# Kernel optimization log

Measured on AMD Instinct MI355X. Metric: run time of the kernel, lower is better.

Reference implementation:

```python
import jax, jax.numpy as jnp
import numpy as np

N = 50000
E = 800000
D_IN = 256
D_OUT = 512
GIN_EPS = 0.0      # eps param, train_eps=False -> constant
BN_EPS = 1e-5      # BatchNorm1d default eps


def setup_inputs() -> dict:
    key = jax.random.key(0)
    ks = jax.random.split(key, 9)
    x = jax.random.normal(ks[0], (N, D_IN), dtype=jnp.float32)
    edge_index = jax.random.randint(ks[1], (2, E), 0, N, dtype=jnp.int32)
    edge_weight = jax.random.uniform(ks[2], (E,), dtype=jnp.float32)
    # MLP params: Linear(D_IN,D_OUT) -> BatchNorm1d(D_OUT) -> ReLU -> Linear(D_OUT,D_OUT)
    s1 = 1.0 / np.sqrt(D_IN)
    s2 = 1.0 / np.sqrt(D_OUT)
    W1 = jax.random.uniform(ks[3], (D_IN, D_OUT), jnp.float32, -s1, s1)
    b1 = jax.random.uniform(ks[4], (D_OUT,), jnp.float32, -s1, s1)
    gamma = jnp.ones((D_OUT,), jnp.float32)
    beta = jnp.zeros((D_OUT,), jnp.float32)
    W2 = jax.random.uniform(ks[5], (D_OUT, D_OUT), jnp.float32, -s2, s2)
    b2 = jax.random.uniform(ks[6], (D_OUT,), jnp.float32, -s2, s2)
    return {"x": x, "edge_index": edge_index, "edge_weight": edge_weight,
            "W1": W1, "b1": b1, "gamma": gamma, "beta": beta, "W2": W2, "b2": b2}


def reference(x, edge_index, edge_weight, W1, b1, gamma, beta, W2, b2):
    row, col = edge_index[0], edge_index[1]
    # gather neighbor features, scale by edge weight, scatter-add into destination rows
    msg = edge_weight[:, None] * x[col]                      # (E, D_IN)
    agg = jax.ops.segment_sum(msg, row, num_segments=x.shape[0])  # (N, D_IN)
    h = (1.0 + GIN_EPS) * x + agg                            # GIN combine
    # MLP: Linear -> BatchNorm1d (training-mode batch stats) -> ReLU -> Linear
    h = h @ W1 + b1                                          # (N, D_OUT)
    mean = jnp.mean(h, axis=0)
    var = jnp.var(h, axis=0)                                 # biased, as torch BN uses
    h = (h - mean) * jax.lax.rsqrt(var + BN_EPS) * gamma + beta
    h = jax.nn.relu(h)
    return h @ W2 + b2
```

## Files before the change

### kernel.cpp

```cpp
#include <hip/hip_runtime.h>

#define NNODES 50000
#define NEDGES 800000
#define DIN    256
#define DOUT   512
#define MP     50048
#define BN_EPS 1e-5f
#define NBLK   196

#define CVT_B  6250
#define ZERO_B 391
#define T1_B   128
#define T2_B   256
#define PREP_B (CVT_B + ZERO_B + T1_B + T2_B)

typedef __attribute__((ext_vector_type(8))) __bf16 bf16x8;
typedef __attribute__((ext_vector_type(4))) float  floatx4;

__device__ __forceinline__ uint pkbf(float a, float b) {
    union { __bf16 h[2]; uint u; } cv;
    cv.h[0] = (__bf16)a; cv.h[1] = (__bf16)b;
    return cv.u;
}
__device__ __forceinline__ ushort f2bf(float f) {
    union { __bf16 h; ushort u; } cv;
    cv.h = (__bf16)f;
    return cv.u;
}
__device__ __forceinline__ float bf2f(ushort b) {
    union { uint u; float f; } v; v.u = ((uint)b) << 16;
    return v.f;
}
__device__ __forceinline__ uint bnpack(uint u, float s0, float s1, float h0, float h1) {
    float a = fmaxf(bf2f((ushort)(u & 0xffff)) * s0 + h0, 0.f);
    float b = fmaxf(bf2f((ushort)(u >> 16))    * s1 + h1, 0.f);
    return pkbf(a, b);
}

__global__ __launch_bounds__(256) void k_prep(const float* __restrict__ x, ushort* __restrict__ xb,
                                              const float* __restrict__ W1, ushort* __restrict__ W1T,
                                              const float* __restrict__ W2, ushort* __restrict__ W2T,
                                              int* __restrict__ zi, float* __restrict__ zf) {
    __shared__ float tile[32][33];
    int b = blockIdx.x;
    int t = threadIdx.x;
    if (b < CVT_B) {
        size_t base = ((size_t)b * 256 + t) * 8;
        float4 v0 = *(const float4*)(x + base);
        float4 v1 = *(const float4*)(x + base + 4);
        uint4 o;
        o.x = pkbf(v0.x, v0.y);
        o.y = pkbf(v0.z, v0.w);
        o.z = pkbf(v1.x, v1.y);
        o.w = pkbf(v1.z, v1.w);
        *(uint4*)(xb + base) = o;
        return;
    }
    b -= CVT_B;
    if (b < ZERO_B) {
        int i = b * 256 + t;
        if (i < 2 * MP) zi[i] = 0;
        if (i < 1024)   zf[i] = 0.f;
        return;
    }
    b -= ZERO_B;
    const float* W; ushort* WT; int K, Nc, bx, by;
    if (b < T1_B) { W = W1; WT = W1T; K = DIN;  Nc = DOUT; bx = b & 15; by = b >> 4; }
    else { b -= T1_B; W = W2; WT = W2T; K = DOUT; Nc = DOUT; bx = b & 15; by = b >> 4; }
    int lx = t & 31, ly = t >> 5;
    #pragma unroll
    for (int p = 0; p < 4; ++p)
        tile[ly + p * 8][lx] = W[(size_t)(by * 32 + ly + p * 8) * Nc + bx * 32 + lx];
    __syncthreads();
    #pragma unroll
    for (int p = 0; p < 4; ++p)
        WT[(size_t)(bx * 32 + ly + p * 8) * K + by * 32 + lx] = f2bf(tile[lx][ly + p * 8]);
}

__global__ void k_count(const int* __restrict__ ei, int* __restrict__ deg) {
    int e = blockIdx.x * 256 + threadIdx.x;
    atomicAdd(&deg[ei[e]], 1);
}

__global__ void k_scan_block(const int* __restrict__ deg, int* __restrict__ rowstart,
                             int* __restrict__ bsum) {
    __shared__ int s[256];
    int t = threadIdx.x;
    int i = blockIdx.x * 256 + t;
    int v = (i < NNODES) ? deg[i] : 0;
    s[t] = v; __syncthreads();
    #pragma unroll
    for (int d = 1; d < 256; d <<= 1) {
        int add = (t >= d) ? s[t - d] : 0;
        __syncthreads();
        s[t] += add;
        __syncthreads();
    }
    if (i < MP) rowstart[i] = s[t] - v;
    if (t == 255) bsum[blockIdx.x] = s[255];
}

__global__ void k_scan_bsum(const int* __restrict__ bsum, int* __restrict__ bofs) {
    __shared__ int s[256];
    int t = threadIdx.x;
    int v = (t < NBLK) ? bsum[t] : 0;
    s[t] = v; __syncthreads();
    #pragma unroll
    for (int d = 1; d < 256; d <<= 1) {
        int add = (t >= d) ? s[t - d] : 0;
        __syncthreads();
        s[t] += add;
        __syncthreads();
    }
    bofs[t] = s[t] - v;
}

__global__ void k_bucket(const int* __restrict__ ei, const float* __restrict__ ew,
                         const int* __restrict__ rowstart, const int* __restrict__ bofs,
                         int* __restrict__ cursor, int2* __restrict__ cw) {
    int e = blockIdx.x * 256 + threadIdx.x;
    int r = ei[e];
    int c = ei[NEDGES + e];
    float w = ew[e];
    int pos = rowstart[r] + bofs[r >> 8] + atomicAdd(&cursor[r], 1);
    cw[pos] = make_int2(c, __float_as_int(w));
}

__global__ __launch_bounds__(256) void k_aggregate(const ushort* __restrict__ xb,
                                                   const int2* __restrict__ cw,
                                                   const int* __restrict__ rowstart,
                                                   const int* __restrict__ bofs,
                                                   const int* __restrict__ deg,
                                                   ushort* __restrict__ h0b) {
    int t = threadIdx.x;
    int wv = t >> 6, lane = t & 63;
    int n = blockIdx.x * 4 + wv;
    if (n >= MP) return;
    ushort* dst = h0b + (size_t)n * DIN + lane * 4;
    if (n >= NNODES) {
        *(ushort4*)dst = make_ushort4(0, 0, 0, 0);
        return;
    }
    const ushort* xl = xb + lane * 4;
    ushort4 sd = *(const ushort4*)(xl + (size_t)n * DIN);
    float4 acc = make_float4(bf2f(sd.x), bf2f(sd.y), bf2f(sd.z), bf2f(sd.w));
    int start = rowstart[n] + bofs[n >> 8];
    int end   = start + deg[n];
    int j = start;
    for (; j + 3 < end; j += 4) {
        int2 e0 = cw[j], e1 = cw[j + 1], e2 = cw[j + 2], e3 = cw[j + 3];
        ushort4 v0 = *(const ushort4*)(xl + (size_t)e0.x * DIN);
        ushort4 v1 = *(const ushort4*)(xl + (size_t)e1.x * DIN);
        ushort4 v2 = *(const ushort4*)(xl + (size_t)e2.x * DIN);
        ushort4 v3 = *(const ushort4*)(xl + (size_t)e3.x * DIN);
        float w0 = __int_as_float(e0.y), w1 = __int_as_float(e1.y);
        float w2 = __int_as_float(e2.y), w3 = __int_as_float(e3.y);
        acc.x += w0 * bf2f(v0.x); acc.y += w0 * bf2f(v0.y); acc.z += w0 * bf2f(v0.z); acc.w += w0 * bf2f(v0.w);
        acc.x += w1 * bf2f(v1.x); acc.y += w1 * bf2f(v1.y); acc.z += w1 * bf2f(v1.z); acc.w += w1 * bf2f(v1.w);
        acc.x += w2 * bf2f(v2.x); acc.y += w2 * bf2f(v2.y); acc.z += w2 * bf2f(v2.z); acc.w += w2 * bf2f(v2.w);
        acc.x += w3 * bf2f(v3.x); acc.y += w3 * bf2f(v3.y); acc.z += w3 * bf2f(v3.z); acc.w += w3 * bf2f(v3.w);
    }
    for (; j < end; ++j) {
        int2 cv = cw[j];
        float w = __int_as_float(cv.y);
        ushort4 v = *(const ushort4*)(xl + (size_t)cv.x * DIN);
        acc.x += w * bf2f(v.x); acc.y += w * bf2f(v.y); acc.z += w * bf2f(v.z); acc.w += w * bf2f(v.w);
    }
    uint2 o;
    o.x = pkbf(acc.x, acc.y);
    o.y = pkbf(acc.z, acc.w);
    *(uint2*)dst = o;
}

template<int KDIM, int MODE>
__global__ __launch_bounds__(256) void k_gemm(const ushort* __restrict__ A,
                                              const ushort* __restrict__ BT,
                                              const float* __restrict__ bias,
                                              const float* __restrict__ scale,
                                              const float* __restrict__ shift,
                                              float* __restrict__ gsum,
                                              float* __restrict__ gsq,
                                              void* __restrict__ out) {
    constexpr int LDSK = 64 + 8;
    __shared__ ushort As[128][LDSK];
    __shared__ ushort Bs[128][LDSK];

    int t    = threadIdx.x;
    int bm   = blockIdx.x >> 2;
    int bn   = blockIdx.x & 3;
    int lane = t & 63;
    int w    = t >> 6;
    int wr   = w >> 1, wc = w & 1;
    int l15  = lane & 15, l4 = lane >> 4;

    floatx4 acc[4][4] = {};

    int arow = t >> 3;
    int acol = (t & 7) * 8;
    const size_t abase = (size_t)(bm * 128) * KDIM;
    const size_t bbase = (size_t)(bn * 128) * KDIM;

    for (int k0 = 0; k0 < KDIM; k0 += 64) {
        float4 sc0, sc1, sh0, sh1;
        if (MODE == 2) {
            sc0 = *(const float4*)(scale + k0 + acol);
            sc1 = *(const float4*)(scale + k0 + acol + 4);
            sh0 = *(const float4*)(shift + k0 + acol);
            sh1 = *(const float4*)(shift + k0 + acol + 4);
        }
        #pragma unroll
        for (int p = 0; p < 4; ++p) {
            int row = p * 32 + arow;
            uint4 va = *(const uint4*)(A  + abase + (size_t)row * KDIM + k0 + acol);
            if (MODE == 2) {
                va.x = bnpack(va.x, sc0.x, sc0.y, sh0.x, sh0.y);
                va.y = bnpack(va.y, sc0.z, sc0.w, sh0.z, sh0.w);
                va.z = bnpack(va.z, sc1.x, sc1.y, sh1.x, sh1.y);
                va.w = bnpack(va.w, sc1.z, sc1.w, sh1.z, sh1.w);
            }
            *(uint4*)&As[row][acol] = va;
            uint4 vb = *(const uint4*)(BT + bbase + (size_t)row * KDIM + k0 + acol);
            *(uint4*)&Bs[row][acol] = vb;
        }
        __syncthreads();
        #pragma unroll
        for (int ks = 0; ks < 2; ++ks) {
            bf16x8 af[4], bfr[4];
            #pragma unroll
            for (int m = 0; m < 4; ++m)
                af[m] = *(const bf16x8*)&As[wr * 64 + m * 16 + l15][ks * 32 + l4 * 8];
            #pragma unroll
            for (int n = 0; n < 4; ++n)
                bfr[n] = *(const bf16x8*)&Bs[wc * 64 + n * 16 + l15][ks * 32 + l4 * 8];
            #pragma unroll
            for (int m = 0; m < 4; ++m)
                #pragma unroll
                for (int n = 0; n < 4; ++n)
                    acc[m][n] = __builtin_amdgcn_mfma_f32_16x16x32_bf16(af[m], bfr[n], acc[m][n], 0, 0, 0);
        }
        __syncthreads();
    }

    float csum[4], csq[4];
    #pragma unroll
    for (int n = 0; n < 4; ++n) { csum[n] = 0.f; csq[n] = 0.f; }

    #pragma unroll
    for (int n = 0; n < 4; ++n) {
        int col = bn * 128 + wc * 64 + n * 16 + l15;
        float bv = bias[col];
        #pragma unroll
        for (int m = 0; m < 4; ++m) {
            int rbase = bm * 128 + wr * 64 + m * 16 + l4 * 4;
            #pragma unroll
            for (int i = 0; i < 4; ++i) {
                int grow = rbase + i;
                float vv = acc[m][n][i] + bv;
                if (MODE == 1) {
                    ((ushort*)out)[(size_t)grow * DOUT + col] = f2bf(vv);
                    if (grow < NNODES) { csum[n] += vv; csq[n] += vv * vv; }
                } else {
                    if (grow < NNODES)
                        ((float*)out)[(size_t)grow * DOUT + col] = vv;
                }
            }
        }
    }

    if (MODE == 1) {
        float* sumarr = (float*)&As[0][0];
        float* sqarr  = sumarr + 1024;
        int cid = wr * 4 + l4;
        #pragma unroll
        for (int n = 0; n < 4; ++n) {
            int colL = wc * 64 + n * 16 + l15;
            sumarr[cid * 128 + colL] = csum[n];
            sqarr [cid * 128 + colL] = csq[n];
        }
        __syncthreads();
        if (t < 128) {
            float s = 0.f, q = 0.f;
            #pragma unroll
            for (int k = 0; k < 8; ++k) { s += sumarr[k * 128 + t]; q += sqarr[k * 128 + t]; }
            atomicAdd(&gsum[bn * 128 + t], s);
            atomicAdd(&gsq [bn * 128 + t], q);
        }
    }
}

__global__ void k_bn_finalize(const float* __restrict__ sum, const float* __restrict__ sumsq,
                              const float* __restrict__ gamma, const float* __restrict__ beta,
                              float* __restrict__ scale, float* __restrict__ shift) {
    int c = threadIdx.x;
    float mean = sum[c] * (1.0f / NNODES);
    float var  = sumsq[c] * (1.0f / NNODES) - mean * mean;
    float sc   = gamma[c] * rsqrtf(var + BN_EPS);
    scale[c] = sc;
    shift[c] = beta[c] - mean * sc;
}

extern "C" void kernel_launch(void* const* d_in, const int* in_sizes, int n_in,
                              void* d_out, int out_size, void* d_ws, size_t ws_size,
                              hipStream_t stream) {
    const float* x     = (const float*)d_in[0];
    const int*   ei    = (const int*)  d_in[1];
    const float* ew    = (const float*)d_in[2];
    const float* W1    = (const float*)d_in[3];
    const float* b1    = (const float*)d_in[4];
    const float* gamma = (const float*)d_in[5];
    const float* beta  = (const float*)d_in[6];
    const float* W2    = (const float*)d_in[7];
    const float* b2    = (const float*)d_in[8];

    char* ws = (char*)d_ws;
    ushort* h1b = (ushort*)ws;                       size_t off = (size_t)MP * DOUT * 2;
    ushort* W1T = (ushort*)(ws + off);               off += (size_t)DOUT * DIN * 2;
    ushort* W2T = (ushort*)(ws + off);               off += (size_t)DOUT * DOUT * 2;
    float* colsum   = (float*)(ws + off);            off += 512 * 4;
    float* colsumsq = (float*)(ws + off);            off += 512 * 4;
    float* scale    = (float*)(ws + off);            off += 512 * 4;
    float* shift    = (float*)(ws + off);            off += 512 * 4;

    char* ob = (char*)d_out;
    ushort* h0b     = (ushort*)ob;                   size_t ooff = (size_t)MP * DIN * 2;
    ushort* xb      = (ushort*)(ob + ooff);          ooff += (size_t)NNODES * DIN * 2;
    int2*   cw      = (int2*)(ob + ooff);            ooff += (size_t)NEDGES * 8;
    int*    deg     = (int*)(ob + ooff);             ooff += (size_t)MP * 4;
    int*    cursor  = (int*)(ob + ooff);             ooff += (size_t)MP * 4;
    int*    rowstart= (int*)(ob + ooff);             ooff += (size_t)MP * 4;
    int*    bsum    = (int*)(ob + ooff);             ooff += 256 * 4;
    int*    bofs    = (int*)(ob + ooff);             ooff += 256 * 4;
    float*  outp    = (float*)d_out;

    k_prep<<<PREP_B, 256, 0, stream>>>(x, xb, W1, W1T, W2, W2T, deg, colsum);

    k_count<<<NEDGES / 256, 256, 0, stream>>>(ei, deg);
    k_scan_block<<<NBLK, 256, 0, stream>>>(deg, rowstart, bsum);
    k_scan_bsum<<<1, 256, 0, stream>>>(bsum, bofs);
    k_bucket<<<NEDGES / 256, 256, 0, stream>>>(ei, ew, rowstart, bofs, cursor, cw);

    k_aggregate<<<MP / 4, 256, 0, stream>>>(xb, cw, rowstart, bofs, deg, h0b);

    k_gemm<DIN, 1><<<(MP / 128) * 4, 256, 0, stream>>>(h0b, W1T, b1, nullptr, nullptr,
                                                       colsum, colsumsq, (void*)h1b);
    k_bn_finalize<<<1, 512, 0, stream>>>(colsum, colsumsq, gamma, beta, scale, shift);
    k_gemm<DOUT, 2><<<(MP / 128) * 4, 256, 0, stream>>>(h1b, W2T, b2, scale, shift,
                                                        nullptr, nullptr, (void*)outp);
}
```

Before: 417.3 us.

## Use direct global-to-LDS loads with XOR swizzle and XCD-aware block remap in GEMM

```diff
diff --git a/kernel.cpp b/kernel.cpp
--- a/kernel.cpp
+++ b/kernel.cpp
@@ -35,6 +35,11 @@
     float a = fmaxf(bf2f((ushort)(u & 0xffff)) * s0 + h0, 0.f);
     float b = fmaxf(bf2f((ushort)(u >> 16))    * s1 + h1, 0.f);
     return pkbf(a, b);
+}
+__device__ __forceinline__ void gload16(const ushort* g, ushort* l) {
+    __builtin_amdgcn_global_load_lds(
+        (const __attribute__((address_space(1))) uint*)g,
+        (__attribute__((address_space(3))) uint*)l, 16, 0, 0);
 }
 
 __global__ __launch_bounds__(256) void k_prep(const float* __restrict__ x, ushort* __restrict__ xb,
@@ -181,57 +186,79 @@
                                               float* __restrict__ gsum,
                                               float* __restrict__ gsq,
                                               void* __restrict__ out) {
-    constexpr int LDSK = 64 + 8;
-    __shared__ ushort As[128][LDSK];
-    __shared__ ushort Bs[128][LDSK];
-
-    int t    = threadIdx.x;
-    int bm   = blockIdx.x >> 2;
-    int bn   = blockIdx.x & 3;
+    constexpr int ALD = (MODE == 1) ? 64 : 72;
+    __shared__ ushort As[128][ALD];
+    __shared__ ushort Bs[128][64];
+
+    int t = threadIdx.x;
+
+    int nwg  = gridDim.x;
+    int q    = nwg >> 3, r = nwg & 7;
+    int xcd  = blockIdx.x & 7, loc = blockIdx.x >> 3;
+    int wgid = (xcd < r ? xcd * (q + 1) : r * (q + 1) + (xcd - r) * q) + loc;
+    int bm   = wgid >> 2;
+    int bn   = wgid & 3;
+
     int lane = t & 63;
-    int w    = t >> 6;
-    int wr   = w >> 1, wc = w & 1;
+    int wv   = t >> 6;
+    int wr   = wv >> 1, wc = wv & 1;
     int l15  = lane & 15, l4 = lane >> 4;
 
-    floatx4 acc[4][4] = {};
+    int rr = lane >> 3;
+    int gs = (lane & 7) ^ rr;
 
     int arow = t >> 3;
     int acol = (t & 7) * 8;
+
+    floatx4 acc[4][4] = {};
     const size_t abase = (size_t)(bm * 128) * KDIM;
     const size_t bbase = (size_t)(bn * 128) * KDIM;
 
     for (int k0 = 0; k0 < KDIM; k0 += 64) {
-        float4 sc0, sc1, sh0, sh1;
-        if (MODE == 2) {
-            sc0 = *(const float4*)(scale + k0 + acol);
-            sc1 = *(const float4*)(scale + k0 + acol + 4);
-            sh0 = *(const float4*)(shift + k0 + acol);
-            sh1 = *(const float4*)(shift + k0 + acol + 4);
-        }
         #pragma unroll
         for (int p = 0; p < 4; ++p) {
-            int row = p * 32 + arow;
-            uint4 va = *(const uint4*)(A  + abase + (size_t)row * KDIM + k0 + acol);
-            if (MODE == 2) {
+            int r0 = p * 32 + wv * 8;
+            gload16(BT + bbase + (size_t)(r0 + rr) * KDIM + k0 + gs * 8, &Bs[r0][0]);
+        }
+        if (MODE == 1) {
+            #pragma unroll
+            for (int p = 0; p < 4; ++p) {
+                int r0 = p * 32 + wv * 8;
+                gload16(A + abase + (size_t)(r0 + rr) * KDIM + k0 + gs * 8, &As[r0][0]);
+            }
+        } else {
+            float4 sc0 = *(const float4*)(scale + k0 + acol);
+            float4 sc1 = *(const float4*)(scale + k0 + acol + 4);
+            float4 sh0 = *(const float4*)(shift + k0 + acol);
+            float4 sh1 = *(const float4*)(shift + k0 + acol + 4);
+            #pragma unroll
+            for (int p = 0; p < 4; ++p) {
+                int row = p * 32 + arow;
+                uint4 va = *(const uint4*)(A + abase + (size_t)row * KDIM + k0 + acol);
                 va.x = bnpack(va.x, sc0.x, sc0.y, sh0.x, sh0.y);
                 va.y = bnpack(va.y, sc0.z, sc0.w, sh0.z, sh0.w);
                 va.z = bnpack(va.z, sc1.x, sc1.y, sh1.x, sh1.y);
                 va.w = bnpack(va.w, sc1.z, sc1.w, sh1.z, sh1.w);
-            }
-            *(uint4*)&As[row][acol] = va;
-            uint4 vb = *(const uint4*)(BT + bbase + (size_t)row * KDIM + k0 + acol);
-            *(uint4*)&Bs[row][acol] = vb;
+                *(uint4*)&As[row][acol] = va;
+            }
         }
         __syncthreads();
         #pragma unroll
         for (int ks = 0; ks < 2; ++ks) {
             bf16x8 af[4], bfr[4];
             #pragma unroll
-            for (int m = 0; m < 4; ++m)
-                af[m] = *(const bf16x8*)&As[wr * 64 + m * 16 + l15][ks * 32 + l4 * 8];
-            #pragma unroll
-            for (int n = 0; n < 4; ++n)
-                bfr[n] = *(const bf16x8*)&Bs[wc * 64 + n * 16 + l15][ks * 32 + l4 * 8];
+            for (int m = 0; m < 4; ++m) {
+                int ar = wr * 64 + m * 16 + l15;
+                if (MODE == 1)
+                    af[m] = *(const bf16x8*)&As[ar][((ks * 4 + l4) ^ (ar & 7)) * 8];
+                else
+                    af[m] = *(const bf16x8*)&As[ar][ks * 32 + l4 * 8];
+            }
+            #pragma unroll
+            for (int n = 0; n < 4; ++n) {
+                int br = wc * 64 + n * 16 + l15;
+                bfr[n] = *(const bf16x8*)&Bs[br][((ks * 4 + l4) ^ (br & 7)) * 8];
+            }
             #pragma unroll
             for (int m = 0; m < 4; ++m)
                 #pragma unroll
@@ -279,11 +306,11 @@
         }
         __syncthreads();
         if (t < 128) {
-            float s = 0.f, q = 0.f;
-            #pragma unroll
-            for (int k = 0; k < 8; ++k) { s += sumarr[k * 128 + t]; q += sqarr[k * 128 + t]; }
+            float s = 0.f, q2 = 0.f;
+            #pragma unroll
+            for (int k = 0; k < 8; ++k) { s += sumarr[k * 128 + t]; q2 += sqarr[k * 128 + t]; }
             atomicAdd(&gsum[bn * 128 + t], s);
-            atomicAdd(&gsq [bn * 128 + t], q);
+            atomicAdd(&gsq [bn * 128 + t], q2);
         }
     }
 }
```

New measurement: 411.7 us. Within noise of the previous version (-1.3%).
